# Kernel tuning notes

Measured on AMD Instinct MI355X. Metric: run time of the kernel, lower is better.

## Reference

```python
import jax, jax.numpy as jnp
import numpy as np

PATCH = 32      # patch_size
OUT = 224       # output_size
K = 9           # num_patches (3x3 grid)
GRID = 3


def _srm_kernel():
    # filter1 + filter2 + filter3 combined (as in SRMConv._get_srm_kernels)
    f = np.array([[-1., 3., -1.], [3., -8., 3.], [-1., 3., -1.]], dtype=np.float32)
    k = np.zeros((3, 3, 3, 3), dtype=np.float32)
    for i in range(3):
        k[i, i] = f
    return jnp.asarray(k)


def setup_inputs() -> dict:
    key = jax.random.key(0)
    x = jax.random.uniform(key, (16, 3, 1024, 1024), dtype=jnp.float32)
    return {"x": x, "srm_kernel": _srm_kernel()}


def reference(x, srm_kernel):
    B, C, H, W = x.shape
    nh, nw = H // PATCH, W // PATCH
    # [N, B, C, P, P], N patches in row-major (i, j) order to match the loop
    p = x.reshape(B, C, nh, PATCH, nw, PATCH).transpose(2, 4, 0, 1, 3, 5)
    p = p.reshape(nh * nw, B, C, PATCH, PATCH)

    dx = jnp.abs(p[..., 1:] - p[..., :-1])
    dy = jnp.abs(p[..., 1:, :] - p[..., :-1, :])
    ax = (1, 2, 3, 4)  # stats over the whole batch, as in the original .item() scoring
    grad_mean = (dx.mean(axis=ax) + dy.mean(axis=ax)) * 0.5
    grad_var = (jnp.var(dx, axis=ax, ddof=1) + jnp.var(dy, axis=ax, ddof=1)) * 0.5
    score = grad_mean * grad_var                      # [N]

    order = jnp.argsort(score)                        # ascending, like np.argsort
    rich = p[order[-K:]]                              # [9, B, C, P, P]
    poor = p[order[:K]]

    def reconstruct(ps):
        # 3x3 grid of PATCH x PATCH patches -> [B, C, 3P, 3P]
        g = ps.reshape(GRID, GRID, B, C, PATCH, PATCH)
        return g.transpose(2, 3, 0, 4, 1, 5).reshape(B, C, GRID * PATCH, GRID * PATCH)

    def upsample(img):
        # bilinear, align_corners=False (half-pixel centers), upsampling so antialias is a no-op
        return jax.image.resize(img, (B, C, OUT, OUT), method='bilinear')

    def srm(img):
        return jax.lax.conv_general_dilated(
            img, srm_kernel, window_strides=(1, 1), padding=((1, 1), (1, 1)),
            dimension_numbers=('NCHW', 'OIHW', 'NCHW'))

    rich_srm = srm(upsample(reconstruct(rich)))       # [B, 3, 224, 224]
    poor_srm = srm(upsample(reconstruct(poor)))
    return jnp.stack([rich_srm, poor_srm])            # [2, B, 3, 224, 224]
```

## Files before the change

### kernel.cpp

```cpp
#include <hip/hip_runtime.h>


#define NSLICE 48
#define IMG    1048576
#define TILE   8

__global__ __launch_bounds__(256) void k_score(const float* __restrict__ x,
                                               double* __restrict__ part) {
  const int ph = blockIdx.x;
  const int s  = blockIdx.y;
  const int t  = threadIdx.x;
  const float* base = x + (size_t)s * IMG + (size_t)ph * 32768 + 4 * t;

  double s1x = 0.0, s2x = 0.0, s1y = 0.0, s2y = 0.0;
  const bool has_d3 = (t & 7) != 7;

#define LD(r) (*(const float4*)(base + (size_t)(r) * 1024))
#define DX(v) { float nx = __shfl_down((v).x, 1);                              \
    float d0 = fabsf((v).y-(v).x), d1 = fabsf((v).z-(v).y),                    \
          d2 = fabsf((v).w-(v).z);                                             \
    float d3 = has_d3 ? fabsf(nx-(v).w) : 0.f;                                 \
    s1x += (double)((d0+d1)+(d2+d3));                                          \
    s2x += (double)((d0*d0+d1*d1)+(d2*d2+d3*d3)); }
#define DY(a,b) { float e0 = fabsf((b).x-(a).x), e1 = fabsf((b).y-(a).y),      \
                        e2 = fabsf((b).z-(a).z), e3 = fabsf((b).w-(a).w);      \
    s1y += (double)((e0+e1)+(e2+e3));                                          \
    s2y += (double)((e0*e0+e1*e1)+(e2*e2+e3*e3)); }

  float4 v0 = LD(0);
  for (int r = 0; r < 32; r += 8) {
    float4 w1 = LD(r + 1), w2 = LD(r + 2), w3 = LD(r + 3), w4 = LD(r + 4);
    float4 w5 = LD(r + 5), w6 = LD(r + 6), w7 = LD(r + 7);
    float4 w8;
    const bool more = (r + 8 < 32);
    if (more) w8 = LD(r + 8);
    DX(v0); DX(w1); DX(w2); DX(w3); DX(w4); DX(w5); DX(w6); DX(w7);
    DY(v0, w1); DY(w1, w2); DY(w2, w3); DY(w3, w4);
    DY(w4, w5); DY(w5, w6); DY(w6, w7);
    if (more) { DY(w7, w8); v0 = w8; }
  }
#undef LD
#undef DX
#undef DY

#pragma unroll
  for (int off = 4; off > 0; off >>= 1) {
    s1x += __shfl_down(s1x, off, 8);
    s2x += __shfl_down(s2x, off, 8);
    s1y += __shfl_down(s1y, off, 8);
    s2y += __shfl_down(s2y, off, 8);
  }
  if ((t & 7) == 0) {
    const int p = ph * 32 + (t >> 3);
    part[(size_t)(0 * NSLICE + s) * 1024 + p] = s1x;
    part[(size_t)(1 * NSLICE + s) * 1024 + p] = s2x;
    part[(size_t)(2 * NSLICE + s) * 1024 + p] = s1y;
    part[(size_t)(3 * NSLICE + s) * 1024 + p] = s2y;
  }
}

__global__ __launch_bounds__(256) void k_finalize(const double* __restrict__ part,
                                                  double* __restrict__ scores) {
  const int p    = blockIdx.x;
  const int t    = threadIdx.x;
  const int q    = t >> 6;
  const int lane = t & 63;

  double v = 0.0;
  if (lane < NSLICE)
    v = part[(size_t)(q * NSLICE + lane) * 1024 + p];

#pragma unroll
  for (int off = 32; off > 0; off >>= 1) v += __shfl_down(v, off);

  __shared__ double S[4];
  if (lane == 0) S[q] = v;
  __syncthreads();

  if (t == 0) {
    const double N = 47616.0;
    double mx = S[0] / N, my = S[2] / N;
    double vx = (S[1] - S[0] * S[0] / N) / (N - 1.0);
    double vy = (S[3] - S[2] * S[2] / N) / (N - 1.0);
    scores[p] = 0.25 * (mx + my) * (vx + vy);
  }
}

__global__ __launch_bounds__(256) void k_rank(const double* __restrict__ scores,
                                              int* __restrict__ sel) {
  __shared__ double sc[1024];
  const int t = threadIdx.x;
  for (int i = t; i < 1024; i += 256) sc[i] = scores[i];
  __syncthreads();

  const int c = blockIdx.x * 32 + (t >> 3);
  const double mine = sc[c];
  int rank = 0;
  for (int j = (t & 7); j < 1024; j += 8) {
    double vj = sc[j];
    rank += (vj < mine) || (vj == mine && j < c);
  }
#pragma unroll
  for (int off = 4; off > 0; off >>= 1) rank += __shfl_down(rank, off, 8);
  if ((t & 7) == 0) {
    if (rank < 9)          sel[9 + rank]    = c;
    else if (rank >= 1015) sel[rank - 1015] = c;
  }
}

__global__ __launch_bounds__(256) void k_output(const float* __restrict__ x,
                                                const int* __restrict__ sel,
                                                float* __restrict__ out) {
  const int ty  = blockIdx.x;
  const int blk = blockIdx.y;
  const int set = blk / 48;
  const int bc  = blk % 48;
  const int y0  = ty * TILE;

  __shared__ int   i0t[224];
  __shared__ float frt[224];
  __shared__ float R[6][97];
  __shared__ float H[6][224];
  __shared__ float U[10][224];
  __shared__ int   selm[9];
  const int t = threadIdx.x;

  if (t < 9) selm[t] = sel[set * 9 + t];
  if (t < 224) {
    int num = 3 * t - 2;
    int i0, fr7;
    if (num < 0) { i0 = 0; fr7 = 0; }
    else {
      i0 = num / 7; fr7 = num - i0 * 7;
      if (i0 >= 95) { i0 = 95; fr7 = 0; }
    }
    i0t[t] = i0;
    frt[t] = (float)fr7 * (1.0f / 7.0f);
  }
  __syncthreads();

  const int Ylo   = max(y0 - 1, 0);
  const int Yhi   = min(y0 + TILE, 223);
  const int sy_lo = i0t[Ylo];
  const int sy_hi = min(i0t[Yhi] + 1, 95);
  const int nrows = sy_hi - sy_lo + 1;

  const float* src = x + (size_t)bc * IMG;
  for (int idx = t; idx < nrows * 96; idx += 256) {
    int ry = idx / 96, xx = idx - ry * 96;
    int sy = sy_lo + ry;
    int gr = sy >> 5, i = sy & 31;
    int gc = xx >> 5, j = xx & 31;
    int pidx = selm[gr * 3 + gc];
    R[ry][xx] = src[(size_t)((pidx >> 5) * 32 + i) * 1024 + (pidx & 31) * 32 + j];
  }
  __syncthreads();

  for (int idx = t; idx < nrows * 224; idx += 256) {
    int r = idx / 224, X = idx - r * 224;
    int ix0 = i0t[X], ix1 = min(ix0 + 1, 95);
    float fx = frt[X];
    float a = R[r][ix0], b = R[r][ix1];
    H[r][X] = a + fx * (b - a);
  }
  __syncthreads();

  for (int idx = t; idx < 10 * 224; idx += 256) {
    int yy = idx / 224, X = idx - yy * 224;
    int Y = y0 - 1 + yy;
    if ((unsigned)Y < 224u) {
      int a = i0t[Y] - sy_lo;
      int b = min(i0t[Y] + 1, 95) - sy_lo;
      float fy = frt[Y];
      float h0 = H[a][X], h1 = H[b][X];
      U[yy][X] = h0 + fy * (h1 - h0);
    }
  }
  __syncthreads();

  const float F[3][3] = {{-1.f, 3.f, -1.f}, {3.f, -8.f, 3.f}, {-1.f, 3.f, -1.f}};
  float* o = out + (size_t)blk * (224 * 224);
  for (int idx = t; idx < TILE * 224; idx += 256) {
    int yy = idx / 224;
    int xx = idx - yy * 224;
    int y  = y0 + yy;
    float acc = 0.f;
#pragma unroll
    for (int dy = 0; dy < 3; ++dy) {
      int Y = y + dy - 1;
      if ((unsigned)Y >= 224u) continue;
      const float* Ur = U[yy + dy];
#pragma unroll
      for (int dx = 0; dx < 3; ++dx) {
        int X = xx + dx - 1;
        if ((unsigned)X >= 224u) continue;
        acc += F[dy][dx] * Ur[X];
      }
    }
    o[(size_t)y * 224 + xx] = acc;
  }
}

extern "C" void kernel_launch(void* const* d_in, const int* in_sizes, int n_in,
                              void* d_out, int out_size, void* d_ws, size_t ws_size,
                              hipStream_t stream) {
  const float* x = (const float*)d_in[0];
  float* out = (float*)d_out;

  double* part   = (double*)d_ws;
  double* scores = (double*)((char*)d_ws + 1572864);
  int*    sel    = (int*)((char*)d_ws + 1581056);

  k_score   <<<dim3(32, 48), 256, 0, stream>>>(x, part);
  k_finalize<<<1024, 256, 0, stream>>>(part, scores);
  k_rank    <<<32, 256, 0, stream>>>(scores, sel);
  k_output  <<<dim3(28, 96), 256, 0, stream>>>(x, sel, out);
}
```

Measured before the change: 67.62 us.

## Double output tile height and use a register sliding-window SRM stencil

Raises the output tile to 16 rows so each block covers twice the output and the grid halves, which lowers the share of halo rows recomputed per block. The SRM convolution now uses its symmetric structure (corners, edges, centre) and slides along 14 consecutive pixels per thread in registers, cutting shared-memory reads and bounds checks. Out-of-range U rows are zero-filled so the stencil needs no row checks. The cost is per-thread strided stores along x, which coalesce less well than before, and fewer blocks to spread across the GPU.

```diff
diff --git a/kernel.cpp b/kernel.cpp
--- a/kernel.cpp
+++ b/kernel.cpp
@@ -3,7 +3,7 @@
 
 #define NSLICE 48
 #define IMG    1048576
-#define TILE   8
+#define TILE   16
 
 __global__ __launch_bounds__(256) void k_score(const float* __restrict__ x,
                                                double* __restrict__ part) {
@@ -119,9 +119,9 @@
 
   __shared__ int   i0t[224];
   __shared__ float frt[224];
-  __shared__ float R[6][97];
-  __shared__ float H[6][224];
-  __shared__ float U[10][224];
+  __shared__ float R[10][97];
+  __shared__ float H[10][225];
+  __shared__ float U[18][225];
   __shared__ int   selm[9];
   const int t = threadIdx.x;
 
@@ -165,7 +165,7 @@
   }
   __syncthreads();
 
-  for (int idx = t; idx < 10 * 224; idx += 256) {
+  for (int idx = t; idx < (TILE + 2) * 224; idx += 256) {
     int yy = idx / 224, X = idx - yy * 224;
     int Y = y0 - 1 + yy;
     if ((unsigned)Y < 224u) {
@@ -174,30 +174,37 @@
       float fy = frt[Y];
       float h0 = H[a][X], h1 = H[b][X];
       U[yy][X] = h0 + fy * (h1 - h0);
+    } else {
+      U[yy][X] = 0.f;
     }
   }
   __syncthreads();
 
-  const float F[3][3] = {{-1.f, 3.f, -1.f}, {3.f, -8.f, 3.f}, {-1.f, 3.f, -1.f}};
-  float* o = out + (size_t)blk * (224 * 224);
-  for (int idx = t; idx < TILE * 224; idx += 256) {
-    int yy = idx / 224;
-    int xx = idx - yy * 224;
-    int y  = y0 + yy;
-    float acc = 0.f;
-#pragma unroll
-    for (int dy = 0; dy < 3; ++dy) {
-      int Y = y + dy - 1;
-      if ((unsigned)Y >= 224u) continue;
-      const float* Ur = U[yy + dy];
-#pragma unroll
-      for (int dx = 0; dx < 3; ++dx) {
-        int X = xx + dx - 1;
-        if ((unsigned)X >= 224u) continue;
-        acc += F[dy][dx] * Ur[X];
-      }
+  {
+    const int yy = t >> 4;
+    const int xs = (t & 15) * 14;
+    const int y  = y0 + yy;
+    float* o = out + (size_t)blk * (224 * 224) + (size_t)y * 224;
+
+    float aP, mP, aC, mC;
+    if (xs > 0) {
+      aP = U[yy][xs - 1] + U[yy + 2][xs - 1];
+      mP = U[yy + 1][xs - 1];
+    } else { aP = 0.f; mP = 0.f; }
+    aC = U[yy][xs] + U[yy + 2][xs];
+    mC = U[yy + 1][xs];
+
+#pragma unroll
+    for (int i = 0; i < 14; ++i) {
+      const int xx = xs + i;
+      float aN, mN;
+      if (xx < 223) {
+        aN = U[yy][xx + 1] + U[yy + 2][xx + 1];
+        mN = U[yy + 1][xx + 1];
+      } else { aN = 0.f; mN = 0.f; }
+      o[xx] = 3.f * (aC + mP + mN) - (aP + aN) - 8.f * mC;
+      aP = aC; aC = aN; mP = mC; mC = mN;
     }
-    o[(size_t)y * 224 + xx] = acc;
   }
 }
 
@@ -214,5 +221,5 @@
   k_score   <<<dim3(32, 48), 256, 0, stream>>>(x, part);
   k_finalize<<<1024, 256, 0, stream>>>(part, scores);
   k_rank    <<<32, 256, 0, stream>>>(scores, sel);
-  k_output  <<<dim3(28, 96), 256, 0, stream>>>(x, sel, out);
-}
+  k_output  <<<dim3(14, 96), 256, 0, stream>>>(x, sel, out);
+}
```

After: 67.99 us. About the same (+0.5%).

## Restructure output kernel to one wavefront per row with register stencil

Applied to the files above, without the earlier changes.

Rewrites k_output so each 64-lane wavefront produces one 224-wide output row. It loads only the three source rows that row needs with float4 loads, then does the bilinear interpolation in registers and the SRM stencil using wavefront shuffles. This removes the shared-memory H/U staging, the lookup tables and several block barriers. In exchange each row reloads its own source rows, so overlapping source rows are read more than once, and the grid grows to 5376 smaller blocks.

```diff
diff --git a/kernel.cpp b/kernel.cpp
--- a/kernel.cpp
+++ b/kernel.cpp
@@ -3,7 +3,6 @@
 
 #define NSLICE 48
 #define IMG    1048576
-#define TILE   8
 
 __global__ __launch_bounds__(256) void k_score(const float* __restrict__ x,
                                                double* __restrict__ part) {
@@ -111,93 +110,107 @@
 __global__ __launch_bounds__(256) void k_output(const float* __restrict__ x,
                                                 const int* __restrict__ sel,
                                                 float* __restrict__ out) {
-  const int ty  = blockIdx.x;
-  const int blk = blockIdx.y;
+  const int gb   = blockIdx.x;
+  const int blk  = gb / 56;
+  const int y0   = (gb % 56) * 4;
+  const int t    = threadIdx.x;
+  const int w    = t >> 6;
+  const int lane = t & 63;
+  const int y    = y0 + w;
+
   const int set = blk / 48;
   const int bc  = blk % 48;
-  const int y0  = ty * TILE;
-
-  __shared__ int   i0t[224];
-  __shared__ float frt[224];
-  __shared__ float R[6][97];
-  __shared__ float H[6][224];
-  __shared__ float U[10][224];
-  __shared__ int   selm[9];
-  const int t = threadIdx.x;
-
-  if (t < 9) selm[t] = sel[set * 9 + t];
-  if (t < 224) {
-    int num = 3 * t - 2;
-    int i0, fr7;
-    if (num < 0) { i0 = 0; fr7 = 0; }
-    else {
-      i0 = num / 7; fr7 = num - i0 * 7;
-      if (i0 >= 95) { i0 = 95; fr7 = 0; }
+
+  __shared__ float S[4][3][96];
+
+  int   ay[3], by[3];
+  float fy[3];
+  bool  vy[3];
+  int s0;
+  {
+    const int Ylo  = max(y - 1, 0);
+    int numl = 3 * Ylo - 2;
+    s0 = numl < 0 ? 0 : min(numl / 7, 95);
+#pragma unroll
+    for (int q = 0; q < 3; ++q) {
+      int Y  = y - 1 + q;
+      vy[q]  = ((unsigned)Y < 224u);
+      int Yc = min(max(Y, 0), 223);
+      int num = 3 * Yc - 2;
+      int i0  = num < 0 ? 0 : num / 7;
+      float fr = num < 0 ? 0.f : (float)(num - 7 * i0) * (1.f / 7.f);
+      if (i0 >= 95) { i0 = 95; fr = 0.f; }
+      ay[q] = i0 - s0;
+      by[q] = min(i0 + 1, 95) - s0;
+      fy[q] = fr;
     }
-    i0t[t] = i0;
-    frt[t] = (float)fr7 * (1.0f / 7.0f);
+  }
+
+  const float* src = x + (size_t)bc * IMG;
+  for (int ii = lane; ii < 72; ii += 64) {
+    int r    = ii / 24;
+    int c4   = (ii % 24) * 4;
+    int srow = min(s0 + r, 95);
+    int gr = srow >> 5, si = srow & 31;
+    int gc = c4 >> 5,   j  = c4 & 31;
+    int pidx = sel[set * 9 + gr * 3 + gc];
+    const float4 v = *(const float4*)&src[(size_t)((pidx >> 5) * 32 + si) * 1024
+                                          + (pidx & 31) * 32 + j];
+    *(float4*)&S[w][r][c4] = v;
   }
   __syncthreads();
 
-  const int Ylo   = max(y0 - 1, 0);
-  const int Yhi   = min(y0 + TILE, 223);
-  const int sy_lo = i0t[Ylo];
-  const int sy_hi = min(i0t[Yhi] + 1, 95);
-  const int nrows = sy_hi - sy_lo + 1;
-
-  const float* src = x + (size_t)bc * IMG;
-  for (int idx = t; idx < nrows * 96; idx += 256) {
-    int ry = idx / 96, xx = idx - ry * 96;
-    int sy = sy_lo + ry;
-    int gr = sy >> 5, i = sy & 31;
-    int gc = xx >> 5, j = xx & 31;
-    int pidx = selm[gr * 3 + gc];
-    R[ry][xx] = src[(size_t)((pidx >> 5) * 32 + i) * 1024 + (pidx & 31) * 32 + j];
-  }
-  __syncthreads();
-
-  for (int idx = t; idx < nrows * 224; idx += 256) {
-    int r = idx / 224, X = idx - r * 224;
-    int ix0 = i0t[X], ix1 = min(ix0 + 1, 95);
-    float fx = frt[X];
-    float a = R[r][ix0], b = R[r][ix1];
-    H[r][X] = a + fx * (b - a);
-  }
-  __syncthreads();
-
-  for (int idx = t; idx < 10 * 224; idx += 256) {
-    int yy = idx / 224, X = idx - yy * 224;
-    int Y = y0 - 1 + yy;
-    if ((unsigned)Y < 224u) {
-      int a = i0t[Y] - sy_lo;
-      int b = min(i0t[Y] + 1, 95) - sy_lo;
-      float fy = frt[Y];
-      float h0 = H[a][X], h1 = H[b][X];
-      U[yy][X] = h0 + fy * (h1 - h0);
+  float A[4], M[4];
+#pragma unroll
+  for (int k = 0; k < 4; ++k) {
+    int xx = lane + (k << 6);
+    int xc = min(xx, 223);
+    int num = 3 * xc - 2;
+    int ix0 = num < 0 ? 0 : num / 7;
+    float fx = num < 0 ? 0.f : (float)(num - 7 * ix0) * (1.f / 7.f);
+    if (ix0 >= 95) { ix0 = 95; fx = 0.f; }
+    int ix1 = min(ix0 + 1, 95);
+
+    float h0a = S[w][0][ix0], h0b = S[w][0][ix1];
+    float h1a = S[w][1][ix0], h1b = S[w][1][ix1];
+    float h2a = S[w][2][ix0], h2b = S[w][2][ix1];
+    float h0 = h0a + fx * (h0b - h0a);
+    float h1 = h1a + fx * (h1b - h1a);
+    float h2 = h2a + fx * (h2b - h2a);
+
+    float U3[3];
+#pragma unroll
+    for (int q = 0; q < 3; ++q) {
+      float ha = (ay[q] == 0) ? h0 : h1;
+      float hb = (by[q] == 0) ? h0 : ((by[q] == 1) ? h1 : h2);
+      U3[q] = vy[q] ? (ha + fy[q] * (hb - ha)) : 0.f;
     }
-  }
-  __syncthreads();
-
-  const float F[3][3] = {{-1.f, 3.f, -1.f}, {3.f, -8.f, 3.f}, {-1.f, 3.f, -1.f}};
-  float* o = out + (size_t)blk * (224 * 224);
-  for (int idx = t; idx < TILE * 224; idx += 256) {
-    int yy = idx / 224;
-    int xx = idx - yy * 224;
-    int y  = y0 + yy;
-    float acc = 0.f;
-#pragma unroll
-    for (int dy = 0; dy < 3; ++dy) {
-      int Y = y + dy - 1;
-      if ((unsigned)Y >= 224u) continue;
-      const float* Ur = U[yy + dy];
-#pragma unroll
-      for (int dx = 0; dx < 3; ++dx) {
-        int X = xx + dx - 1;
-        if ((unsigned)X >= 224u) continue;
-        acc += F[dy][dx] * Ur[X];
-      }
-    }
-    o[(size_t)y * 224 + xx] = acc;
+    A[k] = U3[0] + U3[2];
+    M[k] = U3[1];
+  }
+
+  float* o = out + (size_t)blk * (224 * 224) + (size_t)y * 224;
+#pragma unroll
+  for (int k = 0; k < 4; ++k) {
+    int xx = lane + (k << 6);
+
+    float aL = __shfl_up(A[k], 1);
+    float mL = __shfl_up(M[k], 1);
+    float aP = (k > 0) ? __shfl(A[k - 1], 63) : 0.f;
+    float mP = (k > 0) ? __shfl(M[k - 1], 63) : 0.f;
+    if (lane == 0) { aL = aP; mL = mP; }
+
+    float aR = __shfl_down(A[k], 1);
+    float mR = __shfl_down(M[k], 1);
+    float aN = (k < 3) ? __shfl(A[k + 1], 0) : 0.f;
+    float mN = (k < 3) ? __shfl(M[k + 1], 0) : 0.f;
+    if (lane == 63) { aR = aN; mR = mN; }
+
+    if (xx == 0)   { aL = 0.f; mL = 0.f; }
+    if (xx == 223) { aR = 0.f; mR = 0.f; }
+
+    if (xx < 224)
+      o[xx] = 3.f * (A[k] + mL + mR) - (aL + aR) - 8.f * M[k];
   }
 }
 
@@ -214,5 +227,5 @@
   k_score   <<<dim3(32, 48), 256, 0, stream>>>(x, part);
   k_finalize<<<1024, 256, 0, stream>>>(part, scores);
   k_rank    <<<32, 256, 0, stream>>>(scores, sel);
-  k_output  <<<dim3(28, 96), 256, 0, stream>>>(x, sel, out);
-}
+  k_output  <<<5376, 256, 0, stream>>>(x, sel, out);
+}
```

New measurement: 64.39 us. 1.05x faster.
